# Kernel tuning notes

Hardware: AMD Instinct MI355X
Metric: run time of the kernel (lower is better)

Reference implementation:

```python
import jax, jax.numpy as jnp
import numpy as np

N_NODES = 100000
N_EDGES = 1600000
DIM_IN = 128
DIM_OUT = 128


def setup_inputs() -> dict:
    key = jax.random.key(0)
    k1, k2, k3, k4, k5 = jax.random.split(key, 5)
    x = jax.random.normal(k1, (N_NODES, DIM_IN), dtype=jnp.float32)
    W = jax.random.normal(k2, (DIM_OUT, DIM_IN), dtype=jnp.float32) * (1.0 / np.sqrt(DIM_IN))
    vals = jax.random.uniform(k3, (N_EDGES,), dtype=jnp.float32)
    src = jax.random.randint(k4, (N_EDGES,), 0, N_NODES, dtype=jnp.int32)
    dst = jax.random.randint(k5, (N_EDGES,), 0, N_NODES, dtype=jnp.int32)
    return {"x": x, "W": W, "vals": vals, "src": src, "dst": dst}


def reference(x, W, vals, src, dst):
    # Linear projection (nn.Linear with bias=False): h = x @ W^T  -> [N, dim_out]
    h = jnp.einsum('nd,od->no', x, W)
    # Sparse adjacency SpMM in COO form: out[i] = sum_{e: dst[e]==i} vals[e] * h[src[e]]
    msgs = vals[:, None] * h[src]  # [E, dim_out] irregular gather
    out = jax.ops.segment_sum(msgs, dst, num_segments=N_NODES)  # [N, dim_out] scatter-add
    return out
```

## Files before the change

### kernel.cpp

```cpp
#include <hip/hip_runtime.h>

#define N_NODES 100000
#define N_EDGES 1600000
#define DIM 128

#define NPB 64
#define NBUCK 1563
#define EPB 2048
#define NBLK_E 782
#define NBLK_G 1563

#define OFF_H       0
#define OFF_BCNT    25600000
#define OFF_BBASE   25606272
#define OFF_BCUR    25612544
#define OFF_EPACK   25618816
#define OFF_ROWPTR  38418816
#define WS_NEED     38818944

static __device__ __forceinline__ unsigned short f2bf(float f) {
    union { float f; unsigned u; } a; a.f = f;
    unsigned r = a.u + 0x7fffu + ((a.u >> 16) & 1u);
    return (unsigned short)(r >> 16);
}

static __device__ __forceinline__ float bflo(unsigned b) {
    return __uint_as_float(b << 16);
}
static __device__ __forceinline__ float bfhi(unsigned b) {
    return __uint_as_float(b & 0xffff0000u);
}

__global__ __launch_bounds__(256) void zero_out_kernel(float4* __restrict__ out) {
    int i = blockIdx.x * 256 + threadIdx.x;
    if (i < N_NODES * DIM / 4) out[i] = make_float4(0.f, 0.f, 0.f, 0.f);
}

__global__ __launch_bounds__(256) void zero_bcnt_kernel(int* __restrict__ c) {
    int i = blockIdx.x * 256 + threadIdx.x;
    if (i < NBUCK) c[i] = 0;
}

__global__ __launch_bounds__(256) void bucket_hist_kernel(
        const int* __restrict__ dst, int* __restrict__ bcnt)
{
    __shared__ int lh[NBUCK];
    const int t = threadIdx.x;
    const int e0 = blockIdx.x * EPB;

    for (int i = t; i < NBUCK; i += 256) lh[i] = 0;
    __syncthreads();
#pragma unroll
    for (int r = 0; r < 8; ++r) {
        int e = e0 + (r << 8) + t;
        if (e < N_EDGES) atomicAdd(&lh[dst[e] >> 6], 1);
    }
    __syncthreads();
    const int phase = (blockIdx.x * 613) % NBUCK;
    for (int k = t; k < NBUCK; k += 256) {
        int i = k + phase; if (i >= NBUCK) i -= NBUCK;
        int c = lh[i];
        if (c) atomicAdd(&bcnt[i], c);
    }
}

__global__ __launch_bounds__(256) void bucket_scan_kernel(
        const int* __restrict__ bcnt, int* __restrict__ bbase,
        int* __restrict__ bcur)
{
    __shared__ int wsh[4];
    const int t = threadIdx.x, lane = t & 63, wv = t >> 6;
    int c[8]; int s = 0;
#pragma unroll
    for (int i = 0; i < 8; ++i) {
        int idx = t * 8 + i;
        c[i] = (idx < NBUCK) ? bcnt[idx] : 0;
        s += c[i];
    }
    int v = s;
#pragma unroll
    for (int off = 1; off < 64; off <<= 1) {
        int u = __shfl_up(v, off, 64);
        if (lane >= off) v += u;
    }
    if (lane == 63) wsh[wv] = v;
    __syncthreads();
    int we = 0;
#pragma unroll
    for (int w = 0; w < 4; ++w) we += (w < wv) ? wsh[w] : 0;
    int run = we + (v - s);
#pragma unroll
    for (int i = 0; i < 8; ++i) {
        int idx = t * 8 + i;
        if (idx < NBUCK) { bbase[idx] = run; bcur[idx] = run; }
        run += c[i];
    }
    if (t == 0) bbase[NBUCK] = N_EDGES;
}

#define GR 64
__global__ __launch_bounds__(256) void gemm_fill_kernel(
        const float4* __restrict__ x4,
        const float4* __restrict__ W4,
        unsigned int* __restrict__ hbits,
        const int* __restrict__ src,
        const int* __restrict__ dst,
        const float* __restrict__ vals,
        int* __restrict__ bcur,
        uint2* __restrict__ ep)
{
    __shared__ alignas(16) char smem[51200];
    const int t = threadIdx.x;

    if (blockIdx.x < NBLK_E) {
        int* lh    = (int*)smem;
        int* lbase = (int*)smem + NBUCK;
        const int e0 = blockIdx.x * EPB;

        for (int i = t; i < NBUCK; i += 256) lh[i] = 0;
        __syncthreads();
#pragma unroll
        for (int r = 0; r < 8; ++r) {
            int e = e0 + (r << 8) + t;
            if (e < N_EDGES) atomicAdd(&lh[dst[e] >> 6], 1);
        }
        __syncthreads();
        const int phase = (blockIdx.x * 613) % NBUCK;
        for (int k = t; k < NBUCK; k += 256) {
            int i = k + phase; if (i >= NBUCK) i -= NBUCK;
            int c = lh[i];
            lbase[i] = c ? atomicAdd(&bcur[i], c) : 0;
            lh[i] = 0;
        }
        __syncthreads();
#pragma unroll
        for (int r = 0; r < 8; ++r) {
            int e = e0 + (r << 8) + t;
            if (e < N_EDGES) {
                int d  = dst[e];
                int bk = d >> 6;
                int p  = lbase[bk] + atomicAdd(&lh[bk], 1);
                ep[p] = make_uint2((unsigned)src[e] | ((unsigned)(d & 63) << 17),
                                   __float_as_uint(vals[e]));
            }
        }
        return;
    }

    float (*xs)[68]   = (float(*)[68])smem;
    float (*wsh)[132] = (float(*)[132])(smem + 17408);

    const int tx = t & 15;
    const int ty = t >> 4;
    const int r0 = (blockIdx.x - NBLK_E) * GR;

    float acc[4][8];
#pragma unroll
    for (int i = 0; i < 4; ++i)
#pragma unroll
        for (int j = 0; j < 8; ++j) acc[i][j] = 0.f;

    for (int kc = 0; kc < 2; ++kc) {
#pragma unroll
        for (int i = 0; i < 4; ++i) {
            int linear = t + 256 * i;
            int r  = linear >> 4;
            int k4 = linear & 15;
            float4 v = make_float4(0.f, 0.f, 0.f, 0.f);
            if (r0 + r < N_NODES) v = x4[(size_t)(r0 + r) * 32 + kc * 16 + k4];
            *(float4*)&xs[r][k4 * 4] = v;
        }
#pragma unroll
        for (int i = 0; i < 8; ++i) {
            int linear = t + 256 * i;
            int c  = linear >> 4;
            int k4 = linear & 15;
            float4 v = W4[(size_t)c * 32 + kc * 16 + k4];
            wsh[k4 * 4 + 0][c] = v.x;
            wsh[k4 * 4 + 1][c] = v.y;
            wsh[k4 * 4 + 2][c] = v.z;
            wsh[k4 * 4 + 3][c] = v.w;
        }
        __syncthreads();

#pragma unroll 4
        for (int kk = 0; kk < 64; ++kk) {
            float xf[4], wf[8];
#pragma unroll
            for (int i = 0; i < 4; ++i) xf[i] = xs[ty * 4 + i][kk];
            float4 wlo = *(const float4*)&wsh[kk][tx * 8];
            float4 whi = *(const float4*)&wsh[kk][tx * 8 + 4];
            wf[0] = wlo.x; wf[1] = wlo.y; wf[2] = wlo.z; wf[3] = wlo.w;
            wf[4] = whi.x; wf[5] = whi.y; wf[6] = whi.z; wf[7] = whi.w;
#pragma unroll
            for (int i = 0; i < 4; ++i)
#pragma unroll
                for (int j = 0; j < 8; ++j) acc[i][j] += xf[i] * wf[j];
        }
        __syncthreads();
    }

#pragma unroll
    for (int i = 0; i < 4; ++i) {
        int r = r0 + ty * 4 + i;
        if (r < N_NODES) {
            uint4 u;
            u.x = (unsigned)f2bf(acc[i][0]) | ((unsigned)f2bf(acc[i][1]) << 16);
            u.y = (unsigned)f2bf(acc[i][2]) | ((unsigned)f2bf(acc[i][3]) << 16);
            u.z = (unsigned)f2bf(acc[i][4]) | ((unsigned)f2bf(acc[i][5]) << 16);
            u.w = (unsigned)f2bf(acc[i][6]) | ((unsigned)f2bf(acc[i][7]) << 16);
            *(uint4*)&hbits[(size_t)r * 64 + tx * 4] = u;
        }
    }
}

__global__ __launch_bounds__(256) void reorder_kernel(
        const int* __restrict__ bbase,
        uint2* __restrict__ ep,
        int* __restrict__ row_ptr)
{
    __shared__ int lcnt[NPB];
    const int t = threadIdx.x;
    const int lane = t & 63;
    const int wv = t >> 6;
    const int b = blockIdx.x;

    const int jb = bbase[b];
    const int je = bbase[b + 1];
    const int cnt = je - jb;

    uint2 e[8];
#pragma unroll
    for (int r = 0; r < 8; ++r) {
        int idx = t + (r << 8);
        if (idx < cnt) e[r] = ep[jb + idx];
    }
    if (t < NPB) lcnt[t] = 0;
    __syncthreads();
#pragma unroll
    for (int r = 0; r < 8; ++r) {
        int idx = t + (r << 8);
        if (idx < cnt) atomicAdd(&lcnt[e[r].x >> 17], 1);
    }
    __syncthreads();
    if (wv == 0) {
        int c = lcnt[lane];
        int v = c;
#pragma unroll
        for (int off = 1; off < 64; off <<= 1) {
            int u = __shfl_up(v, off, 64);
            if (lane >= off) v += u;
        }
        int excl = v - c;
        lcnt[lane] = excl;
        int node = b * NPB + lane;
        if (node <= N_NODES) row_ptr[node] = jb + excl;
    }
    __syncthreads();
#pragma unroll
    for (int r = 0; r < 8; ++r) {
        int idx = t + (r << 8);
        if (idx < cnt) {
            int p = atomicAdd(&lcnt[e[r].x >> 17], 1);
            ep[jb + p] = make_uint2(e[r].x & 0x1FFFFu, e[r].y);
        }
    }
}

__global__ __launch_bounds__(256) void gather_bf16_kernel(
        const unsigned int* __restrict__ hbits,
        const int* __restrict__ row_ptr,
        const uint2* __restrict__ ep,
        float2* __restrict__ out2)
{
    const int lane = threadIdx.x & 63;
    const int node = blockIdx.x * 4 + (threadIdx.x >> 6);
    if (node >= N_NODES) return;

    const int jb = row_ptr[node];
    const int je = row_ptr[node + 1];

    float ax0 = 0.f, ay0 = 0.f, ax1 = 0.f, ay1 = 0.f;
    float ax2 = 0.f, ay2 = 0.f, ax3 = 0.f, ay3 = 0.f;
    float ax4 = 0.f, ay4 = 0.f, ax5 = 0.f, ay5 = 0.f;
    float ax6 = 0.f, ay6 = 0.f, ax7 = 0.f, ay7 = 0.f;

    int j = jb;
    if ((j & 1) && j < je) {
        uint2 e0 = ep[j];
        unsigned b0 = hbits[((size_t)e0.x << 6) + lane];
        float v0 = __uint_as_float(e0.y);
        ax0 += v0 * bflo(b0);
        ay0 += v0 * bfhi(b0);
        ++j;
    }
    for (; j + 7 < je; j += 8) {
        uint4 q0 = *(const uint4*)(ep + j);
        uint4 q1 = *(const uint4*)(ep + j + 2);
        uint4 q2 = *(const uint4*)(ep + j + 4);
        uint4 q3 = *(const uint4*)(ep + j + 6);
        unsigned b0 = hbits[((size_t)q0.x << 6) + lane];
        unsigned b1 = hbits[((size_t)q0.z << 6) + lane];
        unsigned b2 = hbits[((size_t)q1.x << 6) + lane];
        unsigned b3 = hbits[((size_t)q1.z << 6) + lane];
        unsigned b4 = hbits[((size_t)q2.x << 6) + lane];
        unsigned b5 = hbits[((size_t)q2.z << 6) + lane];
        unsigned b6 = hbits[((size_t)q3.x << 6) + lane];
        unsigned b7 = hbits[((size_t)q3.z << 6) + lane];
        float v0 = __uint_as_float(q0.y), v1 = __uint_as_float(q0.w);
        float v2 = __uint_as_float(q1.y), v3 = __uint_as_float(q1.w);
        float v4 = __uint_as_float(q2.y), v5 = __uint_as_float(q2.w);
        float v6 = __uint_as_float(q3.y), v7 = __uint_as_float(q3.w);
        ax0 += v0 * bflo(b0); ay0 += v0 * bfhi(b0);
        ax1 += v1 * bflo(b1); ay1 += v1 * bfhi(b1);
        ax2 += v2 * bflo(b2); ay2 += v2 * bfhi(b2);
        ax3 += v3 * bflo(b3); ay3 += v3 * bfhi(b3);
        ax4 += v4 * bflo(b4); ay4 += v4 * bfhi(b4);
        ax5 += v5 * bflo(b5); ay5 += v5 * bfhi(b5);
        ax6 += v6 * bflo(b6); ay6 += v6 * bfhi(b6);
        ax7 += v7 * bflo(b7); ay7 += v7 * bfhi(b7);
    }
    for (; j + 1 < je; j += 2) {
        uint4 q0 = *(const uint4*)(ep + j);
        unsigned b0 = hbits[((size_t)q0.x << 6) + lane];
        unsigned b1 = hbits[((size_t)q0.z << 6) + lane];
        float v0 = __uint_as_float(q0.y), v1 = __uint_as_float(q0.w);
        ax0 += v0 * bflo(b0); ay0 += v0 * bfhi(b0);
        ax1 += v1 * bflo(b1); ay1 += v1 * bfhi(b1);
    }
    if (j < je) {
        uint2 e0 = ep[j];
        unsigned b0 = hbits[((size_t)e0.x << 6) + lane];
        float v0 = __uint_as_float(e0.y);
        ax0 += v0 * bflo(b0);
        ay0 += v0 * bfhi(b0);
    }
    float sx = ((ax0 + ax1) + (ax2 + ax3)) + ((ax4 + ax5) + (ax6 + ax7));
    float sy = ((ay0 + ay1) + (ay2 + ay3)) + ((ay4 + ay5) + (ay6 + ay7));
    out2[(size_t)node * 64 + lane] = make_float2(sx, sy);
}

__global__ __launch_bounds__(256) void gemm_tiled_kernel(
        const float4* __restrict__ x4, const float4* __restrict__ W4,
        unsigned int* __restrict__ hbits)
{
    __shared__ alignas(16) float xs[GR][68];
    __shared__ alignas(16) float wsh[64][132];

    const int t  = threadIdx.x;
    const int tx = t & 15;
    const int ty = t >> 4;
    const int r0 = blockIdx.x * GR;

    float acc[4][8];
#pragma unroll
    for (int i = 0; i < 4; ++i)
#pragma unroll
        for (int j = 0; j < 8; ++j) acc[i][j] = 0.f;

    for (int kc = 0; kc < 2; ++kc) {
#pragma unroll
        for (int i = 0; i < 4; ++i) {
            int linear = t + 256 * i;
            int r  = linear >> 4;
            int k4 = linear & 15;
            float4 v = make_float4(0.f, 0.f, 0.f, 0.f);
            if (r0 + r < N_NODES) v = x4[(size_t)(r0 + r) * 32 + kc * 16 + k4];
            *(float4*)&xs[r][k4 * 4] = v;
        }
#pragma unroll
        for (int i = 0; i < 8; ++i) {
            int linear = t + 256 * i;
            int c  = linear >> 4;
            int k4 = linear & 15;
            float4 v = W4[(size_t)c * 32 + kc * 16 + k4];
            wsh[k4 * 4 + 0][c] = v.x;
            wsh[k4 * 4 + 1][c] = v.y;
            wsh[k4 * 4 + 2][c] = v.z;
            wsh[k4 * 4 + 3][c] = v.w;
        }
        __syncthreads();
#pragma unroll 4
        for (int kk = 0; kk < 64; ++kk) {
            float xf[4], wf[8];
#pragma unroll
            for (int i = 0; i < 4; ++i) xf[i] = xs[ty * 4 + i][kk];
            float4 wlo = *(const float4*)&wsh[kk][tx * 8];
            float4 whi = *(const float4*)&wsh[kk][tx * 8 + 4];
            wf[0] = wlo.x; wf[1] = wlo.y; wf[2] = wlo.z; wf[3] = wlo.w;
            wf[4] = whi.x; wf[5] = whi.y; wf[6] = whi.z; wf[7] = whi.w;
#pragma unroll
            for (int i = 0; i < 4; ++i)
#pragma unroll
                for (int j = 0; j < 8; ++j) acc[i][j] += xf[i] * wf[j];
        }
        __syncthreads();
    }
#pragma unroll
    for (int i = 0; i < 4; ++i) {
        int r = r0 + ty * 4 + i;
        if (r < N_NODES) {
            uint4 u;
            u.x = (unsigned)f2bf(acc[i][0]) | ((unsigned)f2bf(acc[i][1]) << 16);
            u.y = (unsigned)f2bf(acc[i][2]) | ((unsigned)f2bf(acc[i][3]) << 16);
            u.z = (unsigned)f2bf(acc[i][4]) | ((unsigned)f2bf(acc[i][5]) << 16);
            u.w = (unsigned)f2bf(acc[i][6]) | ((unsigned)f2bf(acc[i][7]) << 16);
            *(uint4*)&hbits[(size_t)r * 64 + tx * 4] = u;
        }
    }
}

__global__ __launch_bounds__(256) void scatter_kernel(
        const unsigned int* __restrict__ hbits, const float* __restrict__ vals,
        const int* __restrict__ src, const int* __restrict__ dst,
        float* __restrict__ out)
{
    const int lane = threadIdx.x & 63;
    int e = (blockIdx.x * 256 + threadIdx.x) >> 6;
    if (e >= N_EDGES) return;
    const int   s = src[e];
    const int   d = dst[e];
    const float v = vals[e];
    unsigned b = hbits[(size_t)s * 64 + lane];
    float* op = out + (size_t)d * DIM + lane * 2;
    atomicAdd(op + 0, v * bflo(b));
    atomicAdd(op + 1, v * bfhi(b));
}

extern "C" void kernel_launch(void* const* d_in, const int* in_sizes, int n_in,
                              void* d_out, int out_size, void* d_ws, size_t ws_size,
                              hipStream_t stream) {
    const float* x    = (const float*)d_in[0];
    const float* W    = (const float*)d_in[1];
    const float* vals = (const float*)d_in[2];
    const int*   src  = (const int*)d_in[3];
    const int*   dst  = (const int*)d_in[4];
    float* out = (float*)d_out;

    char* ws = (char*)d_ws;
    unsigned* hbits = (unsigned*)(ws + OFF_H);
    int*   bcnt    = (int*)(ws + OFF_BCNT);
    int*   bbase   = (int*)(ws + OFF_BBASE);
    int*   bcur    = (int*)(ws + OFF_BCUR);
    uint2* ep      = (uint2*)(ws + OFF_EPACK);
    int*   row_ptr = (int*)(ws + OFF_ROWPTR);

    if (ws_size >= (size_t)WS_NEED) {
        zero_bcnt_kernel<<<(NBUCK + 255) / 256, 256, 0, stream>>>(bcnt);
        bucket_hist_kernel<<<NBLK_E, 256, 0, stream>>>(dst, bcnt);
        bucket_scan_kernel<<<1, 256, 0, stream>>>(bcnt, bbase, bcur);
        gemm_fill_kernel<<<NBLK_E + NBLK_G, 256, 0, stream>>>(
            (const float4*)x, (const float4*)W, hbits, src, dst, vals, bcur, ep);
        reorder_kernel<<<NBUCK, 256, 0, stream>>>(bbase, ep, row_ptr);
        gather_bf16_kernel<<<(N_NODES + 3) / 4, 256, 0, stream>>>(
            hbits, row_ptr, ep, (float2*)out);
    } else {
        gemm_tiled_kernel<<<NBLK_G, 256, 0, stream>>>(
            (const float4*)x, (const float4*)W, hbits);
        zero_out_kernel<<<(N_NODES * DIM / 4 + 255) / 256, 256, 0, stream>>>((float4*)out);
        scatter_kernel<<<(N_EDGES * 64 + 255) / 256, 256, 0, stream>>>(
            hbits, vals, src, dst, out);
    }
}
```

Measured before the change: 302.0 us.

## Move projection GEMM to split-bf16 MFMA and separate bucket fill kernel

Replaces the FP32 FMA tiled GEMM, which was fused with the edge bucket fill in one launch, with a dedicated MFMA kernel. The kernel splits x and W into bf16 hi/lo parts and uses three 16x16x32 bf16 MFMAs per tile to approximate FP32 accuracy. The W tile is stored in LDS with an XOR swizzle. The bucket fill becomes its own kernel launched after the GEMM, so the two no longer overlap in a single heterogeneous grid. It also adds 2-byte scattered output stores, which are less coalesced than the old 16-byte stores.

```diff
diff --git a/kernel.cpp b/kernel.cpp
--- a/kernel.cpp
+++ b/kernel.cpp
@@ -18,12 +18,22 @@
 #define OFF_ROWPTR  38418816
 #define WS_NEED     38818944
 
+typedef __attribute__((ext_vector_type(8))) __bf16 bf16x8;
+typedef __attribute__((ext_vector_type(4))) float  f32x4;
+
+union U4B8 { uint4 u; bf16x8 v; };
+union S8B8 { unsigned short s[8]; bf16x8 v; };
+
 static __device__ __forceinline__ unsigned short f2bf(float f) {
     union { float f; unsigned u; } a; a.f = f;
     unsigned r = a.u + 0x7fffu + ((a.u >> 16) & 1u);
     return (unsigned short)(r >> 16);
 }
 
+static __device__ __forceinline__ float bf2f(unsigned short h) {
+    return __uint_as_float((unsigned)h << 16);
+}
+
 static __device__ __forceinline__ float bflo(unsigned b) {
     return __uint_as_float(b << 16);
 }
@@ -39,6 +49,92 @@
 __global__ __launch_bounds__(256) void zero_bcnt_kernel(int* __restrict__ c) {
     int i = blockIdx.x * 256 + threadIdx.x;
     if (i < NBUCK) c[i] = 0;
+}
+
+#define GMR 64
+__global__ __launch_bounds__(256) void gemm_mfma_kernel(
+        const float4* __restrict__ x4,
+        const float4* __restrict__ W4,
+        unsigned short* __restrict__ hb16)
+{
+    __shared__ alignas(16) unsigned whi[128 * 64];
+    __shared__ alignas(16) unsigned wlo[128 * 64];
+
+    const int t    = threadIdx.x;
+    const int lane = t & 63;
+    const int w    = t >> 6;
+    const int r0   = blockIdx.x * GMR;
+
+#pragma unroll
+    for (int i = 0; i < 16; ++i) {
+        int idx = t + 256 * i;
+        int j   = idx >> 5;
+        int c4  = idx & 31;
+        float4 v = W4[idx];
+        unsigned short hx = f2bf(v.x), hy = f2bf(v.y);
+        unsigned short hz = f2bf(v.z), hw = f2bf(v.w);
+        unsigned short lx = f2bf(v.x - bf2f(hx));
+        unsigned short ly = f2bf(v.y - bf2f(hy));
+        unsigned short lz = f2bf(v.z - bf2f(hz));
+        unsigned short lw = f2bf(v.w - bf2f(hw));
+        int d = c4 * 2;
+        int p = d ^ ((j & 7) << 2);
+        int base = j * 64;
+        whi[base + p]     = (unsigned)hx | ((unsigned)hy << 16);
+        whi[base + p + 1] = (unsigned)hz | ((unsigned)hw << 16);
+        wlo[base + p]     = (unsigned)lx | ((unsigned)ly << 16);
+        wlo[base + p + 1] = (unsigned)lz | ((unsigned)lw << 16);
+    }
+    __syncthreads();
+
+    const int arow = r0 + (w << 4) + (lane & 15);
+    const bool rok = arow < N_NODES;
+    const int kg   = lane >> 4;
+
+    f32x4 acc[8];
+#pragma unroll
+    for (int jt = 0; jt < 8; ++jt) acc[jt] = (f32x4)(0.f);
+
+#pragma unroll
+    for (int ks = 0; ks < 4; ++ks) {
+        float4 a0 = make_float4(0.f, 0.f, 0.f, 0.f);
+        float4 a1 = make_float4(0.f, 0.f, 0.f, 0.f);
+        if (rok) {
+            a0 = x4[(size_t)arow * 32 + ks * 8 + kg * 2];
+            a1 = x4[(size_t)arow * 32 + ks * 8 + kg * 2 + 1];
+        }
+        float av[8] = {a0.x, a0.y, a0.z, a0.w, a1.x, a1.y, a1.z, a1.w};
+        S8B8 ahi, alo;
+#pragma unroll
+        for (int e = 0; e < 8; ++e) {
+            unsigned short h = f2bf(av[e]);
+            ahi.s[e] = h;
+            alo.s[e] = f2bf(av[e] - bf2f(h));
+        }
+
+        const int d0 = (ks << 4) + (kg << 2);
+#pragma unroll
+        for (int jt = 0; jt < 8; ++jt) {
+            int j  = (jt << 4) + (lane & 15);
+            int p0 = d0 ^ ((j & 7) << 2);
+            U4B8 bh, bl;
+            bh.u = *(const uint4*)&whi[j * 64 + p0];
+            bl.u = *(const uint4*)&wlo[j * 64 + p0];
+            acc[jt] = __builtin_amdgcn_mfma_f32_16x16x32_bf16(ahi.v, bh.v, acc[jt], 0, 0, 0);
+            acc[jt] = __builtin_amdgcn_mfma_f32_16x16x32_bf16(alo.v, bh.v, acc[jt], 0, 0, 0);
+            acc[jt] = __builtin_amdgcn_mfma_f32_16x16x32_bf16(ahi.v, bl.v, acc[jt], 0, 0, 0);
+        }
+    }
+
+#pragma unroll
+    for (int jt = 0; jt < 8; ++jt) {
+#pragma unroll
+        for (int r = 0; r < 4; ++r) {
+            int node = r0 + (w << 4) + kg * 4 + r;
+            if (node < N_NODES)
+                hb16[(size_t)node * 128 + (jt << 4) + (lane & 15)] = f2bf(acc[jt][r]);
+        }
+    }
 }
 
 __global__ __launch_bounds__(256) void bucket_hist_kernel(
@@ -98,118 +194,41 @@
     if (t == 0) bbase[NBUCK] = N_EDGES;
 }
 
-#define GR 64
-__global__ __launch_bounds__(256) void gemm_fill_kernel(
-        const float4* __restrict__ x4,
-        const float4* __restrict__ W4,
-        unsigned int* __restrict__ hbits,
-        const int* __restrict__ src,
-        const int* __restrict__ dst,
+__global__ __launch_bounds__(256) void bucket_fill_kernel(
+        const int* __restrict__ src, const int* __restrict__ dst,
         const float* __restrict__ vals,
-        int* __restrict__ bcur,
-        uint2* __restrict__ ep)
-{
-    __shared__ alignas(16) char smem[51200];
+        int* __restrict__ bcur, uint2* __restrict__ ep)
+{
+    __shared__ int lh[NBUCK];
+    __shared__ int lbase[NBUCK];
     const int t = threadIdx.x;
-
-    if (blockIdx.x < NBLK_E) {
-        int* lh    = (int*)smem;
-        int* lbase = (int*)smem + NBUCK;
-        const int e0 = blockIdx.x * EPB;
-
-        for (int i = t; i < NBUCK; i += 256) lh[i] = 0;
-        __syncthreads();
-#pragma unroll
-        for (int r = 0; r < 8; ++r) {
-            int e = e0 + (r << 8) + t;
-            if (e < N_EDGES) atomicAdd(&lh[dst[e] >> 6], 1);
-        }
-        __syncthreads();
-        const int phase = (blockIdx.x * 613) % NBUCK;
-        for (int k = t; k < NBUCK; k += 256) {
-            int i = k + phase; if (i >= NBUCK) i -= NBUCK;
-            int c = lh[i];
-            lbase[i] = c ? atomicAdd(&bcur[i], c) : 0;
-            lh[i] = 0;
-        }
-        __syncthreads();
-#pragma unroll
-        for (int r = 0; r < 8; ++r) {
-            int e = e0 + (r << 8) + t;
-            if (e < N_EDGES) {
-                int d  = dst[e];
-                int bk = d >> 6;
-                int p  = lbase[bk] + atomicAdd(&lh[bk], 1);
-                ep[p] = make_uint2((unsigned)src[e] | ((unsigned)(d & 63) << 17),
-                                   __float_as_uint(vals[e]));
-            }
-        }
-        return;
-    }
-
-    float (*xs)[68]   = (float(*)[68])smem;
-    float (*wsh)[132] = (float(*)[132])(smem + 17408);
-
-    const int tx = t & 15;
-    const int ty = t >> 4;
-    const int r0 = (blockIdx.x - NBLK_E) * GR;
-
-    float acc[4][8];
-#pragma unroll
-    for (int i = 0; i < 4; ++i)
-#pragma unroll
-        for (int j = 0; j < 8; ++j) acc[i][j] = 0.f;
-
-    for (int kc = 0; kc < 2; ++kc) {
-#pragma unroll
-        for (int i = 0; i < 4; ++i) {
-            int linear = t + 256 * i;
-            int r  = linear >> 4;
-            int k4 = linear & 15;
-            float4 v = make_float4(0.f, 0.f, 0.f, 0.f);
-            if (r0 + r < N_NODES) v = x4[(size_t)(r0 + r) * 32 + kc * 16 + k4];
-            *(float4*)&xs[r][k4 * 4] = v;
-        }
-#pragma unroll
-        for (int i = 0; i < 8; ++i) {
-            int linear = t + 256 * i;
-            int c  = linear >> 4;
-            int k4 = linear & 15;
-            float4 v = W4[(size_t)c * 32 + kc * 16 + k4];
-            wsh[k4 * 4 + 0][c] = v.x;
-            wsh[k4 * 4 + 1][c] = v.y;
-            wsh[k4 * 4 + 2][c] = v.z;
-            wsh[k4 * 4 + 3][c] = v.w;
-        }
-        __syncthreads();
-
-#pragma unroll 4
-        for (int kk = 0; kk < 64; ++kk) {
-            float xf[4], wf[8];
-#pragma unroll
-            for (int i = 0; i < 4; ++i) xf[i] = xs[ty * 4 + i][kk];
-            float4 wlo = *(const float4*)&wsh[kk][tx * 8];
-            float4 whi = *(const float4*)&wsh[kk][tx * 8 + 4];
-            wf[0] = wlo.x; wf[1] = wlo.y; wf[2] = wlo.z; wf[3] = wlo.w;
-            wf[4] = whi.x; wf[5] = whi.y; wf[6] = whi.z; wf[7] = whi.w;
-#pragma unroll
-            for (int i = 0; i < 4; ++i)
-#pragma unroll
-                for (int j = 0; j < 8; ++j) acc[i][j] += xf[i] * wf[j];
-        }
-        __syncthreads();
-    }
-
-#pragma unroll
-    for (int i = 0; i < 4; ++i) {
-        int r = r0 + ty * 4 + i;
-        if (r < N_NODES) {
-            uint4 u;
-            u.x = (unsigned)f2bf(acc[i][0]) | ((unsigned)f2bf(acc[i][1]) << 16);
-            u.y = (unsigned)f2bf(acc[i][2]) | ((unsigned)f2bf(acc[i][3]) << 16);
-            u.z = (unsigned)f2bf(acc[i][4]) | ((unsigned)f2bf(acc[i][5]) << 16);
-            u.w = (unsigned)f2bf(acc[i][6]) | ((unsigned)f2bf(acc[i][7]) << 16);
-            *(uint4*)&hbits[(size_t)r * 64 + tx * 4] = u;
+    const int e0 = blockIdx.x * EPB;
+
+    for (int i = t; i < NBUCK; i += 256) lh[i] = 0;
+    __syncthreads();
+#pragma unroll
+    for (int r = 0; r < 8; ++r) {
+        int e = e0 + (r << 8) + t;
+        if (e < N_EDGES) atomicAdd(&lh[dst[e] >> 6], 1);
+    }
+    __syncthreads();
+    const int phase = (blockIdx.x * 613) % NBUCK;
+    for (int k = t; k < NBUCK; k += 256) {
+        int i = k + phase; if (i >= NBUCK) i -= NBUCK;
+        int c = lh[i];
+        lbase[i] = c ? atomicAdd(&bcur[i], c) : 0;
+        lh[i] = 0;
+    }
+    __syncthreads();
+#pragma unroll
+    for (int r = 0; r < 8; ++r) {
+        int e = e0 + (r << 8) + t;
+        if (e < N_EDGES) {
+            int d  = dst[e];
+            int bk = d >> 6;
+            int p  = lbase[bk] + atomicAdd(&lh[bk], 1);
+            ep[p] = make_uint2((unsigned)src[e] | ((unsigned)(d & 63) << 17),
+                               __float_as_uint(vals[e]));
         }
     }
 }
@@ -340,6 +359,7 @@
     out2[(size_t)node * 64 + lane] = make_float2(sx, sy);
 }
 
+#define GR 64
 __global__ __launch_bounds__(256) void gemm_tiled_kernel(
         const float4* __restrict__ x4, const float4* __restrict__ W4,
         unsigned int* __restrict__ hbits)
@@ -385,10 +405,10 @@
             float xf[4], wf[8];
 #pragma unroll
             for (int i = 0; i < 4; ++i) xf[i] = xs[ty * 4 + i][kk];
-            float4 wlo = *(const float4*)&wsh[kk][tx * 8];
-            float4 whi = *(const float4*)&wsh[kk][tx * 8 + 4];
-            wf[0] = wlo.x; wf[1] = wlo.y; wf[2] = wlo.z; wf[3] = wlo.w;
-            wf[4] = whi.x; wf[5] = whi.y; wf[6] = whi.z; wf[7] = whi.w;
+            float4 wlo4 = *(const float4*)&wsh[kk][tx * 8];
+            float4 whi4 = *(const float4*)&wsh[kk][tx * 8 + 4];
+            wf[0] = wlo4.x; wf[1] = wlo4.y; wf[2] = wlo4.z; wf[3] = wlo4.w;
+            wf[4] = whi4.x; wf[5] = whi4.y; wf[6] = whi4.z; wf[7] = whi4.w;
 #pragma unroll
             for (int i = 0; i < 4; ++i)
 #pragma unroll
@@ -449,8 +469,9 @@
         zero_bcnt_kernel<<<(NBUCK + 255) / 256, 256, 0, stream>>>(bcnt);
         bucket_hist_kernel<<<NBLK_E, 256, 0, stream>>>(dst, bcnt);
         bucket_scan_kernel<<<1, 256, 0, stream>>>(bcnt, bbase, bcur);
-        gemm_fill_kernel<<<NBLK_E + NBLK_G, 256, 0, stream>>>(
-            (const float4*)x, (const float4*)W, hbits, src, dst, vals, bcur, ep);
+        gemm_mfma_kernel<<<NBLK_G, 256, 0, stream>>>(
+            (const float4*)x, (const float4*)W, (unsigned short*)hbits);
+        bucket_fill_kernel<<<NBLK_E, 256, 0, stream>>>(src, dst, vals, bcur, ep);
         reorder_kernel<<<NBUCK, 256, 0, stream>>>(bbase, ep, row_ptr);
         gather_bf16_kernel<<<(N_NODES + 3) / 4, 256, 0, stream>>>(
             hbits, row_ptr, ep, (float2*)out);
```

Measured after the change: 289.0 us. -4.3%, faster.
